# Optimization experiments

Hardware: AMD Instinct MI355X
Metric: run time of the kernel (lower is better)

## Reference

```python
import jax, jax.numpy as jnp
import numpy as np

B, S, H, NH = 4, 2048, 1024, 16
HD = H // NH  # head_size = 64


def setup_inputs() -> dict:
    key = jax.random.key(0)
    ks = jax.random.split(key, 12)
    s = 1.0 / np.sqrt(H)
    return {
        "query": jax.random.normal(ks[0], (B, S, H), jnp.float32),
        "key": jax.random.normal(ks[1], (B, S, H), jnp.float32),
        "value": jax.random.normal(ks[2], (B, S, H), jnp.float32),
        "attention_mask": jax.random.randint(ks[3], (B, 1, S, S), 0, 2).astype(jnp.float32),
        "Wq": jax.random.normal(ks[4], (H, H), jnp.float32) * s,
        "bq": jnp.zeros((H,), jnp.float32),
        "Wk": jax.random.normal(ks[5], (H, H), jnp.float32) * s,
        "bk": jnp.zeros((H,), jnp.float32),
        "Wv": jax.random.normal(ks[6], (H, H), jnp.float32) * s,
        "bv": jnp.zeros((H,), jnp.float32),
        "Wo": jax.random.normal(ks[7], (H, H), jnp.float32) * s,
        "bo": jnp.zeros((H,), jnp.float32),
    }


def reference(query, key, value, attention_mask, Wq, bq, Wk, bk, Wv, bv, Wo, bo):
    # Linear projections (weights stored [in, out])
    q = query @ Wq + bq   # [B, S, H]
    k = key @ Wk + bk
    v = value @ Wv + bv
    # split heads -> [B, NH, S, HD]
    def heads(x):
        return x.reshape(B, -1, NH, HD).transpose(0, 2, 1, 3)
    q, k, v = heads(q), heads(k), heads(v)
    scale = 1.0 / np.sqrt(HD)
    scores = jnp.einsum("bhqd,bhkd->bhqk", q, k) * scale  # [B, NH, S, S]
    scores = scores + attention_mask * (-1e9)
    attn = jax.nn.softmax(scores, axis=-1)
    # dropout is identity in eval mode (deterministic reference)
    out = jnp.einsum("bhqk,bhkd->bhqd", attn, v)  # [B, NH, S, HD]
    out = out.transpose(0, 2, 1, 3).reshape(B, -1, H)  # [B, S, H]
    return out @ Wo + bo
```

## Files before the change

### kernel.cpp

```cpp
#include <hip/hip_runtime.h>
#include <hip/hip_bf16.h>
#include <stdint.h>

#define B_ 4
#define S_ 2048
#define H_ 1024
#define NH_ 16
#define HD_ 64

typedef __attribute__((ext_vector_type(8))) short short8;
typedef __attribute__((ext_vector_type(4))) float f32x4;
typedef __attribute__((ext_vector_type(4))) unsigned short ushort4v;

__device__ __forceinline__ unsigned short f2bf(float f) {
  union { float f; unsigned u; } x; x.f = f;
  unsigned r = x.u + 0x7fffu + ((x.u >> 16) & 1u);
  return (unsigned short)(r >> 16);
}

#define ALDS16(g, l) \
  __builtin_amdgcn_global_load_lds((const __attribute__((address_space(1))) void*)(g), \
                                   (__attribute__((address_space(3))) void*)(l), 16, 0, 0)

__global__ __launch_bounds__(256) void cvt_in(
    const float* __restrict__ q, const float* __restrict__ k, const float* __restrict__ v,
    unsigned short* __restrict__ oq, unsigned short* __restrict__ ok2, unsigned short* __restrict__ ov) {
  const int z = blockIdx.z;
  const float* src = z == 0 ? q : (z == 1 ? k : v);
  unsigned short* dst = z == 0 ? oq : (z == 1 ? ok2 : ov);
  const size_t i = ((size_t)blockIdx.x * 256 + threadIdx.x) * 8;
  const f32x4 a = *reinterpret_cast<const f32x4*>(src + i);
  const f32x4 c = *reinterpret_cast<const f32x4*>(src + i + 4);
  short8 o;
#pragma unroll
  for (int j = 0; j < 4; ++j) { o[j] = (short)f2bf(a[j]); o[j + 4] = (short)f2bf(c[j]); }
  *reinterpret_cast<short8*>(dst + i) = o;
}

__global__ __launch_bounds__(256) void packmask(
    const float* __restrict__ mask, unsigned long long* __restrict__ mb) {
  const int w = threadIdx.x >> 6, lane = threadIdx.x & 63;
  const int wbase = (blockIdx.x * 4 + w) * 32;
#pragma unroll 8
  for (int i = 0; i < 32; ++i) {
    const float v = mask[(size_t)(wbase + i) * 64 + lane];
    const unsigned long long bits = __ballot(v == 0.0f);
    if (lane == 0) mb[wbase + i] = bits;
  }
}

__global__ __launch_bounds__(256) void cvt_w(
    const float* __restrict__ Wq, const float* __restrict__ Wk,
    const float* __restrict__ Wv, const float* __restrict__ Wo,
    unsigned short* __restrict__ wt) {
  __shared__ float tile[64][65];
  const int z = blockIdx.z;
  const float* W = z == 0 ? Wq : (z == 1 ? Wk : (z == 2 ? Wv : Wo));
  unsigned short* out = wt + (size_t)z * H_ * H_;
  const int t = threadIdx.x;
  const int r0 = blockIdx.y * 64, c0 = blockIdx.x * 64;
  const int tr = t >> 4, tc = (t & 15) * 4;
#pragma unroll
  for (int rr = 0; rr < 4; ++rr) {
    const int row = rr * 16 + tr;
    const f32x4 val = *reinterpret_cast<const f32x4*>(W + (size_t)(r0 + row) * H_ + c0 + tc);
#pragma unroll
    for (int j = 0; j < 4; ++j) tile[row][tc + j] = val[j];
  }
  __syncthreads();
#pragma unroll
  for (int rr = 0; rr < 4; ++rr) {
    const int c = rr * 16 + tr;
    ushort4v o;
#pragma unroll
    for (int j = 0; j < 4; ++j) o[j] = f2bf(tile[tc + j][c]);
    *reinterpret_cast<ushort4v*>(out + (size_t)(c0 + c) * H_ + r0 + tc) = o;
  }
}

template <int OUTMODE>
__device__ __forceinline__ void gemm_body(
    const unsigned short* __restrict__ X, const unsigned short* __restrict__ Wt,
    const float* __restrict__ bias, float oscale, unsigned short* __restrict__ obf,
    float* __restrict__ of32) {
  __shared__ unsigned short As[128 * 64];
  __shared__ unsigned short Bs[128 * 64];
  const int t = threadIdx.x;
  const int w = t >> 6, l = t & 63;
  const int lr = l & 15, lg = l >> 4;
  const int brow = blockIdx.x * 128, bcol = blockIdx.y * 128;
  const int wr = (w >> 1) * 64, wc = (w & 1) * 64;
  f32x4 acc[4][4] = {};
  const unsigned short* xb = X + (size_t)brow * 1024;
  const unsigned short* wb = Wt + (size_t)bcol * 1024;
  int srow[4], skl[4];
#pragma unroll
  for (int j = 0; j < 4; ++j) {
    const int c = t + j * 256;
    srow[j] = c >> 3;
    skl[j] = ((c & 7) ^ ((c >> 3) & 7)) * 8;
  }
  for (int kt = 0; kt < 1024; kt += 64) {
#pragma unroll
    for (int j = 0; j < 4; ++j) {
      ALDS16(xb + (size_t)srow[j] * 1024 + kt + skl[j], As + (t + j * 256) * 8);
      ALDS16(wb + (size_t)srow[j] * 1024 + kt + skl[j], Bs + (t + j * 256) * 8);
    }
    __syncthreads();
#pragma unroll
    for (int kk = 0; kk < 2; ++kk) {
      short8 af[4], bf[4];
#pragma unroll
      for (int m = 0; m < 4; ++m) {
        const int ra = wr + m * 16 + lr;
        af[m] = *reinterpret_cast<const short8*>(As + ra * 64 + ((kk * 4 + lg) ^ (ra & 7)) * 8);
      }
#pragma unroll
      for (int n = 0; n < 4; ++n) {
        const int rb = wc + n * 16 + lr;
        bf[n] = *reinterpret_cast<const short8*>(Bs + rb * 64 + ((kk * 4 + lg) ^ (rb & 7)) * 8);
      }
#pragma unroll
      for (int m = 0; m < 4; ++m)
#pragma unroll
        for (int n = 0; n < 4; ++n)
          acc[m][n] = __builtin_amdgcn_mfma_f32_16x16x32_bf16(af[m], bf[n], acc[m][n], 0, 0, 0);
    }
    __syncthreads();
  }
#pragma unroll
  for (int m = 0; m < 4; ++m) {
#pragma unroll
    for (int n = 0; n < 4; ++n) {
#pragma unroll
      for (int r = 0; r < 4; ++r) {
        const int gr = brow + wr + m * 16 + lg * 4 + r;
        const int gc = bcol + wc + n * 16 + lr;
        const float val = (acc[m][n][r] + bias[gc]) * oscale;
        if (OUTMODE == 0) {
          const int bb = gr >> 11, ss = gr & 2047, hh = gc >> 6, dd = gc & 63;
          obf[(((size_t)(bb * NH_ + hh)) * S_ + ss) * HD_ + dd] = f2bf(val);
        } else {
          of32[(size_t)gr * H_ + gc] = val;
        }
      }
    }
  }
}

#define QSCL 0.1803368801111244f

__global__ __launch_bounds__(256, 4) void gemm_qkv(
    const unsigned short* __restrict__ xq, const unsigned short* __restrict__ xk,
    const unsigned short* __restrict__ xv, const unsigned short* __restrict__ wt,
    const float* __restrict__ bq, const float* __restrict__ bk, const float* __restrict__ bv,
    unsigned short* __restrict__ qh, unsigned short* __restrict__ kh,
    unsigned short* __restrict__ vh) {
  const int z = blockIdx.z;
  const unsigned short* X = z == 0 ? xq : (z == 1 ? xk : xv);
  const unsigned short* W = wt + (size_t)z * H_ * H_;
  const float* bias = z == 0 ? bq : (z == 1 ? bk : bv);
  unsigned short* out = z == 0 ? qh : (z == 1 ? kh : vh);
  const float scl = z == 0 ? QSCL : 1.0f;
  gemm_body<0>(X, W, bias, scl, out, nullptr);
}

__global__ __launch_bounds__(256, 4) void gemm_out(
    const unsigned short* __restrict__ ao, const unsigned short* __restrict__ wt,
    const float* __restrict__ bo, float* __restrict__ out) {
  gemm_body<1>(ao, wt, bo, 1.0f, nullptr, out);
}

__global__ __launch_bounds__(256) void vtrans(
    const unsigned short* __restrict__ vh, unsigned short* __restrict__ vt) {
  __shared__ unsigned short tile[64 * 72];
  const int bh = blockIdx.y;
  const int s0 = blockIdx.x * 64;
  const int t = threadIdx.x;
  const unsigned short* src = vh + (size_t)bh * S_ * HD_ + (size_t)s0 * HD_;
#pragma unroll
  for (int r = 0; r < 2; ++r) {
    const int i = t + r * 256;
    const int row = i >> 3, kc = i & 7;
    const short8 v = *reinterpret_cast<const short8*>(src + row * 64 + kc * 8);
    *reinterpret_cast<short8*>(tile + row * 72 + kc * 8) = v;
  }
  __syncthreads();
  unsigned short* dst = vt + (size_t)bh * HD_ * S_;
#pragma unroll
  for (int r = 0; r < 2; ++r) {
    const int i = t + r * 256;
    const int d = i >> 3, sc = i & 7;
    short8 o;
#pragma unroll
    for (int j = 0; j < 8; ++j) o[j] = (short)tile[(sc * 8 + j) * 72 + d];
    *reinterpret_cast<short8*>(dst + (size_t)d * S_ + s0 + sc * 8) = o;
  }
}

__global__ __launch_bounds__(256, 2) void attn_kernel(
    const unsigned short* __restrict__ qh, const unsigned short* __restrict__ kh,
    const unsigned short* __restrict__ vt, const unsigned long long* __restrict__ mb,
    unsigned short* __restrict__ ao) {
  __shared__ unsigned short Ks[2][64 * 64];
  __shared__ unsigned short Vs[2][64 * 64];
  __shared__ unsigned short Ps[4][16 * 64 * 3];
  const int t = threadIdx.x, w = t >> 6, l = t & 63;
  const int lr = l & 15, lg = l >> 4;
  const int flat = blockIdx.x;
  const int g = flat >> 9;
  const int x = flat & 511;
  const int bh = g * 32 + (x & 7) * 4 + (x >> 7);
  const int qt = (x >> 3) & 15;
  const int b = bh >> 4, h = bh & 15;
  const unsigned short* qptr = qh + (size_t)bh * S_ * HD_;
  const unsigned short* kptr = kh + (size_t)bh * S_ * HD_;
  const unsigned short* vptr = vt + (size_t)bh * HD_ * S_;
  const unsigned long long* mbase = mb + (size_t)b * S_ * (S_ / 64);
  const int qbase = qt * 128 + w * 32;

  short8 qf[2][2];
#pragma unroll
  for (int qs = 0; qs < 2; ++qs) {
    const unsigned short* qp = qptr + (size_t)(qbase + qs * 16 + lr) * HD_ + lg * 8;
    qf[qs][0] = *reinterpret_cast<const short8*>(qp);
    qf[qs][1] = *reinterpret_cast<const short8*>(qp + 32);
  }
  short8 ones;
#pragma unroll
  for (int jj = 0; jj < 8; ++jj) ones[jj] = (short)0x3F80;

  const int si0 = t, si1 = t + 256;
  const int srow0 = si0 >> 3, sk0 = ((si0 & 7) ^ (srow0 & 7)) * 8;
  const int srow1 = si1 >> 3, sk1 = ((si1 & 7) ^ (srow1 & 7)) * 8;
  const unsigned short* ksrc0 = kptr + (size_t)srow0 * HD_ + sk0;
  const unsigned short* ksrc1 = kptr + (size_t)srow1 * HD_ + sk1;
  const unsigned short* vsrc0 = vptr + (size_t)srow0 * S_ + sk0;
  const unsigned short* vsrc1 = vptr + (size_t)srow1 * S_ + sk1;
  size_t moff[2][4];
#pragma unroll
  for (int qs = 0; qs < 2; ++qs)
#pragma unroll
    for (int r = 0; r < 4; ++r)
      moff[qs][r] = (size_t)(qbase + qs * 16 + lg * 4 + r) * (S_ / 64);

  ALDS16(ksrc0, Ks[0] + si0 * 8);
  ALDS16(ksrc1, Ks[0] + si1 * 8);
  ALDS16(vsrc0, Vs[0] + si0 * 8);
  ALDS16(vsrc1, Vs[0] + si1 * 8);
  __syncthreads();

  f32x4 acc_o[2][4] = {};
  f32x4 acc_l[2] = {};
  unsigned short* pw = Ps[w];
  int cur = 0;

  for (int kv = 0; kv < S_; kv += 64) {
    unsigned msel[2][4][4];
#pragma unroll
    for (int qs = 0; qs < 2; ++qs)
#pragma unroll
      for (int r = 0; r < 4; ++r) {
        const unsigned long long mwv = mbase[moff[qs][r] + (kv >> 6)];
        const unsigned long long sh = mwv >> lr;
        const unsigned lo = (unsigned)sh, hi = (unsigned)(sh >> 32);
        msel[qs][r][0] = 0u - (lo & 1u);
        msel[qs][r][1] = 0u - ((lo >> 16) & 1u);
        msel[qs][r][2] = 0u - (hi & 1u);
        msel[qs][r][3] = 0u - ((hi >> 16) & 1u);
      }

    const int nkv = (kv + 64 < S_) ? kv + 64 : 0;
    ALDS16(ksrc0 + (size_t)nkv * HD_, Ks[cur ^ 1] + si0 * 8);
    ALDS16(ksrc1 + (size_t)nkv * HD_, Ks[cur ^ 1] + si1 * 8);
    ALDS16(vsrc0 + nkv, Vs[cur ^ 1] + si0 * 8);
    ALDS16(vsrc1 + nkv, Vs[cur ^ 1] + si1 * 8);

    float p[2][4][4];
#pragma unroll
    for (int n = 0; n < 4; ++n) {
      const int krow = n * 16 + lr;
      const short8 kf0 = *reinterpret_cast<const short8*>(Ks[cur] + krow * 64 + ((0 + lg) ^ (krow & 7)) * 8);
      const short8 kf1 = *reinterpret_cast<const short8*>(Ks[cur] + krow * 64 + ((4 + lg) ^ (krow & 7)) * 8);
#pragma unroll
      for (int qs = 0; qs < 2; ++qs) {
        f32x4 sc = {};
        sc = __builtin_amdgcn_mfma_f32_16x16x32_bf16(qf[qs][0], kf0, sc, 0, 0, 0);
        sc = __builtin_amdgcn_mfma_f32_16x16x32_bf16(qf[qs][1], kf1, sc, 0, 0, 0);
#pragma unroll
        for (int r = 0; r < 4; ++r) {
          union { float f; unsigned u; } cv;
          cv.f = __builtin_amdgcn_exp2f(sc[r]);
          cv.u &= msel[qs][r][n];
          p[qs][n][r] = cv.f;
        }
      }
    }

    short8 pf[2][2];
#pragma unroll
    for (int qs = 0; qs < 2; ++qs) {
#pragma unroll
      for (int r = 0; r < 4; ++r) {
        const int row = lg * 4 + r;
#pragma unroll
        for (int n = 0; n < 4; ++n) {
          union { float f; unsigned u; } cv; cv.f = p[qs][n][r];
          const int col = n * 16 + lr;
          pw[row * 64 + ((col >> 3) ^ (row & 7)) * 8 + (col & 7)] = (unsigned short)(cv.u >> 16);
        }
      }
      pf[qs][0] = *reinterpret_cast<const short8*>(pw + lr * 64 + ((0 + lg) ^ (lr & 7)) * 8);
      pf[qs][1] = *reinterpret_cast<const short8*>(pw + lr * 64 + ((4 + lg) ^ (lr & 7)) * 8);
      acc_l[qs] = __builtin_amdgcn_mfma_f32_16x16x32_bf16(pf[qs][0], ones, acc_l[qs], 0, 0, 0);
      acc_l[qs] = __builtin_amdgcn_mfma_f32_16x16x32_bf16(pf[qs][1], ones, acc_l[qs], 0, 0, 0);
    }

    __builtin_amdgcn_s_setprio(1);
#pragma unroll
    for (int d = 0; d < 4; ++d) {
      const int vrow = d * 16 + lr;
      const short8 vf0 = *reinterpret_cast<const short8*>(Vs[cur] + vrow * 64 + ((0 + lg) ^ (vrow & 7)) * 8);
      const short8 vf1 = *reinterpret_cast<const short8*>(Vs[cur] + vrow * 64 + ((4 + lg) ^ (vrow & 7)) * 8);
#pragma unroll
      for (int qs = 0; qs < 2; ++qs) {
        acc_o[qs][d] = __builtin_amdgcn_mfma_f32_16x16x32_bf16(pf[qs][0], vf0, acc_o[qs][d], 0, 0, 0);
        acc_o[qs][d] = __builtin_amdgcn_mfma_f32_16x16x32_bf16(pf[qs][1], vf1, acc_o[qs][d], 0, 0, 0);
      }
    }
    __builtin_amdgcn_s_setprio(0);
    __syncthreads();
    cur ^= 1;
  }

#pragma unroll
  for (int qs = 0; qs < 2; ++qs)
#pragma unroll
    for (int r = 0; r < 4; ++r) {
      const float inv = __builtin_amdgcn_rcpf(acc_l[qs][r]);
      const int qrow = qbase + qs * 16 + lg * 4 + r;
      unsigned short* orow = ao + ((size_t)b * S_ + qrow) * H_ + h * HD_;
#pragma unroll
      for (int d = 0; d < 4; ++d)
        orow[d * 16 + lr] = f2bf(acc_o[qs][d][r] * inv);
    }
}

extern "C" void kernel_launch(void* const* d_in, const int* in_sizes, int n_in,
                              void* d_out, int out_size, void* d_ws, size_t ws_size,
                              hipStream_t stream) {
  (void)in_sizes; (void)n_in; (void)out_size; (void)ws_size;
  const float* query = (const float*)d_in[0];
  const float* key_  = (const float*)d_in[1];
  const float* value = (const float*)d_in[2];
  const float* mask  = (const float*)d_in[3];
  const float* Wq = (const float*)d_in[4];
  const float* bq = (const float*)d_in[5];
  const float* Wk = (const float*)d_in[6];
  const float* bk = (const float*)d_in[7];
  const float* Wv = (const float*)d_in[8];
  const float* bv = (const float*)d_in[9];
  const float* Wo = (const float*)d_in[10];
  const float* bo = (const float*)d_in[11];
  float* out = (float*)d_out;

  char* ws = (char*)d_ws;
  const size_t MB16 = (size_t)1 << 24;
  unsigned short* XQ = (unsigned short*)(ws + 0 * MB16);
  unsigned short* XK = (unsigned short*)(ws + 1 * MB16);
  unsigned short* XV = (unsigned short*)(ws + 2 * MB16);
  unsigned short* QH = (unsigned short*)(ws + 3 * MB16);
  unsigned short* KH = (unsigned short*)(ws + 4 * MB16);
  unsigned short* VH = (unsigned short*)(ws + 5 * MB16);
  unsigned short* WT = (unsigned short*)(ws + 6 * MB16);
  unsigned long long* MBits = (unsigned long long*)(ws + 6 * MB16 + (size_t)4 * H_ * H_ * 2);
  unsigned short* AO = XQ;
  unsigned short* VT = XK;

  cvt_in<<<dim3(4096, 1, 3), 256, 0, stream>>>(query, key_, value, XQ, XK, XV);
  packmask<<<dim3(2048), 256, 0, stream>>>(mask, MBits);
  cvt_w<<<dim3(16, 16, 4), 256, 0, stream>>>(Wq, Wk, Wv, Wo, WT);
  gemm_qkv<<<dim3(64, 8, 3), 256, 0, stream>>>(XQ, XK, XV, WT, bq, bk, bv, QH, KH, VH);
  vtrans<<<dim3(32, 64), 256, 0, stream>>>(VH, VT);
  attn_kernel<<<dim3(1024), 256, 0, stream>>>(QH, KH, VT, MBits, AO);
  gemm_out<<<dim3(64, 8, 1), 256, 0, stream>>>(AO, WT + 3 * (size_t)H_ * H_, bo, out);
}
```

Measured before the change: 266.2 us.

## Triple-buffer K/V tiles in attention with two-ahead prefetch and partial vmcnt wait

The attention kernel moves from double to triple buffering of its K and V LDS tiles. Each tile is now prefetched two iterations ahead, and the full __syncthreads is replaced by an s_waitcnt vmcnt(4) plus barrier, so the newest prefetch can stay in flight across the barrier. The oversized P scratch buffer is cut to one third, which keeps total LDS use unchanged and so does not reduce occupancy. The aim is to hide global-to-LDS load latency better, at the cost of relying on exact vmcnt ordering, since the mask loads are also counted as vector memory operations.

```diff
diff --git a/kernel.cpp b/kernel.cpp
--- a/kernel.cpp
+++ b/kernel.cpp
@@ -202,9 +202,9 @@
     const unsigned short* __restrict__ qh, const unsigned short* __restrict__ kh,
     const unsigned short* __restrict__ vt, const unsigned long long* __restrict__ mb,
     unsigned short* __restrict__ ao) {
-  __shared__ unsigned short Ks[2][64 * 64];
-  __shared__ unsigned short Vs[2][64 * 64];
-  __shared__ unsigned short Ps[4][16 * 64 * 3];
+  __shared__ unsigned short Ks[3][64 * 64];
+  __shared__ unsigned short Vs[3][64 * 64];
+  __shared__ unsigned short Ps[4][16 * 64];
   const int t = threadIdx.x, w = t >> 6, l = t & 63;
   const int lr = l & 15, lg = l >> 4;
   const int flat = blockIdx.x;
@@ -248,7 +248,13 @@
   ALDS16(ksrc1, Ks[0] + si1 * 8);
   ALDS16(vsrc0, Vs[0] + si0 * 8);
   ALDS16(vsrc1, Vs[0] + si1 * 8);
-  __syncthreads();
+  ALDS16(ksrc0 + (size_t)64 * HD_, Ks[1] + si0 * 8);
+  ALDS16(ksrc1 + (size_t)64 * HD_, Ks[1] + si1 * 8);
+  ALDS16(vsrc0 + 64, Vs[1] + si0 * 8);
+  ALDS16(vsrc1 + 64, Vs[1] + si1 * 8);
+  asm volatile("s_waitcnt vmcnt(4)");
+  __builtin_amdgcn_s_barrier();
+  __builtin_amdgcn_sched_barrier(0);
 
   f32x4 acc_o[2][4] = {};
   f32x4 acc_l[2] = {};
@@ -270,18 +276,22 @@
         msel[qs][r][3] = 0u - ((hi >> 16) & 1u);
       }
 
-    const int nkv = (kv + 64 < S_) ? kv + 64 : 0;
-    ALDS16(ksrc0 + (size_t)nkv * HD_, Ks[cur ^ 1] + si0 * 8);
-    ALDS16(ksrc1 + (size_t)nkv * HD_, Ks[cur ^ 1] + si1 * 8);
-    ALDS16(vsrc0 + nkv, Vs[cur ^ 1] + si0 * 8);
-    ALDS16(vsrc1 + nkv, Vs[cur ^ 1] + si1 * 8);
+    const int stb = (cur == 0) ? 2 : cur - 1;
+    const int nkv = (kv + 128 < S_) ? kv + 128 : kv + 128 - S_;
+    ALDS16(ksrc0 + (size_t)nkv * HD_, Ks[stb] + si0 * 8);
+    ALDS16(ksrc1 + (size_t)nkv * HD_, Ks[stb] + si1 * 8);
+    ALDS16(vsrc0 + nkv, Vs[stb] + si0 * 8);
+    ALDS16(vsrc1 + nkv, Vs[stb] + si1 * 8);
+
+    const unsigned short* Kc = Ks[cur];
+    const unsigned short* Vc = Vs[cur];
 
     float p[2][4][4];
 #pragma unroll
     for (int n = 0; n < 4; ++n) {
       const int krow = n * 16 + lr;
-      const short8 kf0 = *reinterpret_cast<const short8*>(Ks[cur] + krow * 64 + ((0 + lg) ^ (krow & 7)) * 8);
-      const short8 kf1 = *reinterpret_cast<const short8*>(Ks[cur] + krow * 64 + ((4 + lg) ^ (krow & 7)) * 8);
+      const short8 kf0 = *reinterpret_cast<const short8*>(Kc + krow * 64 + ((0 + lg) ^ (krow & 7)) * 8);
+      const short8 kf1 = *reinterpret_cast<const short8*>(Kc + krow * 64 + ((4 + lg) ^ (krow & 7)) * 8);
 #pragma unroll
       for (int qs = 0; qs < 2; ++qs) {
         f32x4 sc = {};
@@ -320,8 +330,8 @@
 #pragma unroll
     for (int d = 0; d < 4; ++d) {
       const int vrow = d * 16 + lr;
-      const short8 vf0 = *reinterpret_cast<const short8*>(Vs[cur] + vrow * 64 + ((0 + lg) ^ (vrow & 7)) * 8);
-      const short8 vf1 = *reinterpret_cast<const short8*>(Vs[cur] + vrow * 64 + ((4 + lg) ^ (vrow & 7)) * 8);
+      const short8 vf0 = *reinterpret_cast<const short8*>(Vc + vrow * 64 + ((0 + lg) ^ (vrow & 7)) * 8);
+      const short8 vf1 = *reinterpret_cast<const short8*>(Vc + vrow * 64 + ((4 + lg) ^ (vrow & 7)) * 8);
 #pragma unroll
       for (int qs = 0; qs < 2; ++qs) {
         acc_o[qs][d] = __builtin_amdgcn_mfma_f32_16x16x32_bf16(pf[qs][0], vf0, acc_o[qs][d], 0, 0, 0);
@@ -329,8 +339,11 @@
       }
     }
     __builtin_amdgcn_s_setprio(0);
-    __syncthreads();
-    cur ^= 1;
+
+    asm volatile("s_waitcnt vmcnt(4)");
+    __builtin_amdgcn_s_barrier();
+    __builtin_amdgcn_sched_barrier(0);
+    cur = (cur == 2) ? 0 : cur + 1;
   }
 
 #pragma unroll
```

After: 267.6 us. About the same (+0.5%).

## Fuse V transpose into V projection epilogue and halve attention query tile

Applied to the files above, without the earlier changes.

The V projection now gets its own GEMM launch whose epilogue writes V directly in transposed [B,NH,HD,S] layout using 4-wide stores, which removes the separate vtrans kernel and one round trip of V through memory. The attention kernel drops from 32 to 16 query rows per wave (64 per block), doubling the grid to 2048 blocks, shrinking the P scratch buffer, and raising the launch-bounds occupancy hint to 4. The block-to-head mapping is reworked so that consecutive blocks spread across XCDs. The trade-off is that each K/V tile loaded into LDS is now reused by fewer query rows, so K/V traffic per unit of work doubles.

```diff
diff --git a/kernel.cpp b/kernel.cpp
--- a/kernel.cpp
+++ b/kernel.cpp
@@ -132,16 +132,25 @@
   for (int m = 0; m < 4; ++m) {
 #pragma unroll
     for (int n = 0; n < 4; ++n) {
-#pragma unroll
-      for (int r = 0; r < 4; ++r) {
-        const int gr = brow + wr + m * 16 + lg * 4 + r;
-        const int gc = bcol + wc + n * 16 + lr;
-        const float val = (acc[m][n][r] + bias[gc]) * oscale;
-        if (OUTMODE == 0) {
-          const int bb = gr >> 11, ss = gr & 2047, hh = gc >> 6, dd = gc & 63;
-          obf[(((size_t)(bb * NH_ + hh)) * S_ + ss) * HD_ + dd] = f2bf(val);
-        } else {
-          of32[(size_t)gr * H_ + gc] = val;
+      const int gr0 = brow + wr + m * 16 + lg * 4;
+      const int gc = bcol + wc + n * 16 + lr;
+      if (OUTMODE == 2) {
+        ushort4v o;
+#pragma unroll
+        for (int r = 0; r < 4; ++r) o[r] = f2bf((acc[m][n][r] + bias[gc]) * oscale);
+        const int bb = gr0 >> 11, ss = gr0 & 2047, hh = gc >> 6, dd = gc & 63;
+        *reinterpret_cast<ushort4v*>(obf + ((size_t)(bb * NH_ + hh) * HD_ + dd) * S_ + ss) = o;
+      } else {
+#pragma unroll
+        for (int r = 0; r < 4; ++r) {
+          const int gr = gr0 + r;
+          const float val = (acc[m][n][r] + bias[gc]) * oscale;
+          if (OUTMODE == 0) {
+            const int bb = gr >> 11, ss = gr & 2047, hh = gc >> 6, dd = gc & 63;
+            obf[(((size_t)(bb * NH_ + hh)) * S_ + ss) * HD_ + dd] = f2bf(val);
+          } else {
+            of32[(size_t)gr * H_ + gc] = val;
+          }
         }
       }
     }
@@ -152,17 +161,22 @@
 
 __global__ __launch_bounds__(256, 4) void gemm_qkv(
     const unsigned short* __restrict__ xq, const unsigned short* __restrict__ xk,
-    const unsigned short* __restrict__ xv, const unsigned short* __restrict__ wt,
-    const float* __restrict__ bq, const float* __restrict__ bk, const float* __restrict__ bv,
-    unsigned short* __restrict__ qh, unsigned short* __restrict__ kh,
-    unsigned short* __restrict__ vh) {
+    const unsigned short* __restrict__ wt,
+    const float* __restrict__ bq, const float* __restrict__ bk,
+    unsigned short* __restrict__ qh, unsigned short* __restrict__ kh) {
   const int z = blockIdx.z;
-  const unsigned short* X = z == 0 ? xq : (z == 1 ? xk : xv);
+  const unsigned short* X = z == 0 ? xq : xk;
   const unsigned short* W = wt + (size_t)z * H_ * H_;
-  const float* bias = z == 0 ? bq : (z == 1 ? bk : bv);
-  unsigned short* out = z == 0 ? qh : (z == 1 ? kh : vh);
+  const float* bias = z == 0 ? bq : bk;
+  unsigned short* out = z == 0 ? qh : kh;
   const float scl = z == 0 ? QSCL : 1.0f;
   gemm_body<0>(X, W, bias, scl, out, nullptr);
+}
+
+__global__ __launch_bounds__(256, 4) void gemm_v(
+    const unsigned short* __restrict__ xv, const unsigned short* __restrict__ wt,
+    const float* __restrict__ bv, unsigned short* __restrict__ vtv) {
+  gemm_body<2>(xv, wt + (size_t)2 * H_ * H_, bv, 1.0f, vtv, nullptr);
 }
 
 __global__ __launch_bounds__(256, 4) void gemm_out(
@@ -171,60 +185,33 @@
   gemm_body<1>(ao, wt, bo, 1.0f, nullptr, out);
 }
 
-__global__ __launch_bounds__(256) void vtrans(
-    const unsigned short* __restrict__ vh, unsigned short* __restrict__ vt) {
-  __shared__ unsigned short tile[64 * 72];
-  const int bh = blockIdx.y;
-  const int s0 = blockIdx.x * 64;
-  const int t = threadIdx.x;
-  const unsigned short* src = vh + (size_t)bh * S_ * HD_ + (size_t)s0 * HD_;
-#pragma unroll
-  for (int r = 0; r < 2; ++r) {
-    const int i = t + r * 256;
-    const int row = i >> 3, kc = i & 7;
-    const short8 v = *reinterpret_cast<const short8*>(src + row * 64 + kc * 8);
-    *reinterpret_cast<short8*>(tile + row * 72 + kc * 8) = v;
-  }
-  __syncthreads();
-  unsigned short* dst = vt + (size_t)bh * HD_ * S_;
-#pragma unroll
-  for (int r = 0; r < 2; ++r) {
-    const int i = t + r * 256;
-    const int d = i >> 3, sc = i & 7;
-    short8 o;
-#pragma unroll
-    for (int j = 0; j < 8; ++j) o[j] = (short)tile[(sc * 8 + j) * 72 + d];
-    *reinterpret_cast<short8*>(dst + (size_t)d * S_ + s0 + sc * 8) = o;
-  }
-}
-
-__global__ __launch_bounds__(256, 2) void attn_kernel(
+__global__ __launch_bounds__(256, 4) void attn_kernel(
     const unsigned short* __restrict__ qh, const unsigned short* __restrict__ kh,
     const unsigned short* __restrict__ vt, const unsigned long long* __restrict__ mb,
     unsigned short* __restrict__ ao) {
   __shared__ unsigned short Ks[2][64 * 64];
   __shared__ unsigned short Vs[2][64 * 64];
-  __shared__ unsigned short Ps[4][16 * 64 * 3];
+  __shared__ unsigned short Ps[4][16 * 64];
   const int t = threadIdx.x, w = t >> 6, l = t & 63;
   const int lr = l & 15, lg = l >> 4;
   const int flat = blockIdx.x;
-  const int g = flat >> 9;
-  const int x = flat & 511;
-  const int bh = g * 32 + (x & 7) * 4 + (x >> 7);
-  const int qt = (x >> 3) & 15;
+  const int xcd = flat & 7;
+  const int gen = flat >> 10;
+  const int hh = (flat >> 8) & 3;
+  const int qt = (flat >> 3) & 31;
+  const int bh = gen * 32 + xcd * 4 + hh;
   const int b = bh >> 4, h = bh & 15;
   const unsigned short* qptr = qh + (size_t)bh * S_ * HD_;
   const unsigned short* kptr = kh + (size_t)bh * S_ * HD_;
   const unsigned short* vptr = vt + (size_t)bh * HD_ * S_;
   const unsigned long long* mbase = mb + (size_t)b * S_ * (S_ / 64);
-  const int qbase = qt * 128 + w * 32;
-
-  short8 qf[2][2];
-#pragma unroll
-  for (int qs = 0; qs < 2; ++qs) {
-    const unsigned short* qp = qptr + (size_t)(qbase + qs * 16 + lr) * HD_ + lg * 8;
-    qf[qs][0] = *reinterpret_cast<const short8*>(qp);
-    qf[qs][1] = *reinterpret_cast<const short8*>(qp + 32);
+  const int qbase = qt * 64 + w * 16;
+
+  short8 qf[2];
+  {
+    const unsigned short* qp = qptr + (size_t)(qbase + lr) * HD_ + lg * 8;
+    qf[0] = *reinterpret_cast<const short8*>(qp);
+    qf[1] = *reinterpret_cast<const short8*>(qp + 32);
   }
   short8 ones;
 #pragma unroll
@@ -237,12 +224,10 @@
   const unsigned short* ksrc1 = kptr + (size_t)srow1 * HD_ + sk1;
   const unsigned short* vsrc0 = vptr + (size_t)srow0 * S_ + sk0;
   const unsigned short* vsrc1 = vptr + (size_t)srow1 * S_ + sk1;
-  size_t moff[2][4];
-#pragma unroll
-  for (int qs = 0; qs < 2; ++qs)
-#pragma unroll
-    for (int r = 0; r < 4; ++r)
-      moff[qs][r] = (size_t)(qbase + qs * 16 + lg * 4 + r) * (S_ / 64);
+  size_t moff[4];
+#pragma unroll
+  for (int r = 0; r < 4; ++r)
+    moff[r] = (size_t)(qbase + lg * 4 + r) * (S_ / 64);
 
   ALDS16(ksrc0, Ks[0] + si0 * 8);
   ALDS16(ksrc1, Ks[0] + si1 * 8);
@@ -250,25 +235,23 @@
   ALDS16(vsrc1, Vs[0] + si1 * 8);
   __syncthreads();
 
-  f32x4 acc_o[2][4] = {};
-  f32x4 acc_l[2] = {};
+  f32x4 acc_o[4] = {};
+  f32x4 acc_l = {};
   unsigned short* pw = Ps[w];
   int cur = 0;
 
   for (int kv = 0; kv < S_; kv += 64) {
-    unsigned msel[2][4][4];
-#pragma unroll
-    for (int qs = 0; qs < 2; ++qs)
-#pragma unroll
-      for (int r = 0; r < 4; ++r) {
-        const unsigned long long mwv = mbase[moff[qs][r] + (kv >> 6)];
-        const unsigned long long sh = mwv >> lr;
-        const unsigned lo = (unsigned)sh, hi = (unsigned)(sh >> 32);
-        msel[qs][r][0] = 0u - (lo & 1u);
-        msel[qs][r][1] = 0u - ((lo >> 16) & 1u);
-        msel[qs][r][2] = 0u - (hi & 1u);
-        msel[qs][r][3] = 0u - ((hi >> 16) & 1u);
-      }
+    unsigned msel[4][4];
+#pragma unroll
+    for (int r = 0; r < 4; ++r) {
+      const unsigned long long mwv = mbase[moff[r] + (kv >> 6)];
+      const unsigned long long sh = mwv >> lr;
+      const unsigned lo = (unsigned)sh, hi = (unsigned)(sh >> 32);
+      msel[r][0] = 0u - (lo & 1u);
+      msel[r][1] = 0u - ((lo >> 16) & 1u);
+      msel[r][2] = 0u - (hi & 1u);
+      msel[r][3] = 0u - ((hi >> 16) & 1u);
+    }
 
     const int nkv = (kv + 64 < S_) ? kv + 64 : 0;
     ALDS16(ksrc0 + (size_t)nkv * HD_, Ks[cur ^ 1] + si0 * 8);
@@ -276,57 +259,50 @@
     ALDS16(vsrc0 + nkv, Vs[cur ^ 1] + si0 * 8);
     ALDS16(vsrc1 + nkv, Vs[cur ^ 1] + si1 * 8);
 
-    float p[2][4][4];
+    const unsigned short* Kc = Ks[cur];
+    const unsigned short* Vc = Vs[cur];
+
+    float p[4][4];
 #pragma unroll
     for (int n = 0; n < 4; ++n) {
       const int krow = n * 16 + lr;
-      const short8 kf0 = *reinterpret_cast<const short8*>(Ks[cur] + krow * 64 + ((0 + lg) ^ (krow & 7)) * 8);
-      const short8 kf1 = *reinterpret_cast<const short8*>(Ks[cur] + krow * 64 + ((4 + lg) ^ (krow & 7)) * 8);
-#pragma unroll
-      for (int qs = 0; qs < 2; ++qs) {
-        f32x4 sc = {};
-        sc = __builtin_amdgcn_mfma_f32_16x16x32_bf16(qf[qs][0], kf0, sc, 0, 0, 0);
-        sc = __builtin_amdgcn_mfma_f32_16x16x32_bf16(qf[qs][1], kf1, sc, 0, 0, 0);
-#pragma unroll
-        for (int r = 0; r < 4; ++r) {
-          union { float f; unsigned u; } cv;
-          cv.f = __builtin_amdgcn_exp2f(sc[r]);
-          cv.u &= msel[qs][r][n];
-          p[qs][n][r] = cv.f;
-        }
-      }
-    }
-
-    short8 pf[2][2];
-#pragma unroll
-    for (int qs = 0; qs < 2; ++qs) {
+      const short8 kf0 = *reinterpret_cast<const short8*>(Kc + krow * 64 + ((0 + lg) ^ (krow & 7)) * 8);
+      const short8 kf1 = *reinterpret_cast<const short8*>(Kc + krow * 64 + ((4 + lg) ^ (krow & 7)) * 8);
+      f32x4 sc = {};
+      sc = __builtin_amdgcn_mfma_f32_16x16x32_bf16(qf[0], kf0, sc, 0, 0, 0);
+      sc = __builtin_amdgcn_mfma_f32_16x16x32_bf16(qf[1], kf1, sc, 0, 0, 0);
 #pragma unroll
       for (int r = 0; r < 4; ++r) {
-        const int row = lg * 4 + r;
-#pragma unroll
-        for (int n = 0; n < 4; ++n) {
-          union { float f; unsigned u; } cv; cv.f = p[qs][n][r];
-          const int col = n * 16 + lr;
-          pw[row * 64 + ((col >> 3) ^ (row & 7)) * 8 + (col & 7)] = (unsigned short)(cv.u >> 16);
-        }
-      }
-      pf[qs][0] = *reinterpret_cast<const short8*>(pw + lr * 64 + ((0 + lg) ^ (lr & 7)) * 8);
-      pf[qs][1] = *reinterpret_cast<const short8*>(pw + lr * 64 + ((4 + lg) ^ (lr & 7)) * 8);
-      acc_l[qs] = __builtin_amdgcn_mfma_f32_16x16x32_bf16(pf[qs][0], ones, acc_l[qs], 0, 0, 0);
-      acc_l[qs] = __builtin_amdgcn_mfma_f32_16x16x32_bf16(pf[qs][1], ones, acc_l[qs], 0, 0, 0);
-    }
+        union { float f; unsigned u; } cv;
+        cv.f = __builtin_amdgcn_exp2f(sc[r]);
+        cv.u &= msel[r][n];
+        p[n][r] = cv.f;
+      }
+    }
+
+#pragma unroll
+    for (int r = 0; r < 4; ++r) {
+      const int row = lg * 4 + r;
+#pragma unroll
+      for (int n = 0; n < 4; ++n) {
+        union { float f; unsigned u; } cv; cv.f = p[n][r];
+        const int col = n * 16 + lr;
+        pw[row * 64 + ((col >> 3) ^ (row & 7)) * 8 + (col & 7)] = (unsigned short)(cv.u >> 16);
+      }
+    }
+    short8 pf0 = *reinterpret_cast<const short8*>(pw + lr * 64 + ((0 + lg) ^ (lr & 7)) * 8);
+    short8 pf1 = *reinterpret_cast<const short8*>(pw + lr * 64 + ((4 + lg) ^ (lr & 7)) * 8);
+    acc_l = __builtin_amdgcn_mfma_f32_16x16x32_bf16(pf0, ones, acc_l, 0, 0, 0);
+    acc_l = __builtin_amdgcn_mfma_f32_16x16x32_bf16(pf1, ones, acc_l, 0, 0, 0);
 
     __builtin_amdgcn_s_setprio(1);
 #pragma unroll
     for (int d = 0; d < 4; ++d) {
       const int vrow = d * 16 + lr;
-      const short8 vf0 = *reinterpret_cast<const short8*>(Vs[cur] + vrow * 64 + ((0 + lg) ^ (vrow & 7)) * 8);
-      const short8 vf1 = *reinterpret_cast<const short8*>(Vs[cur] + vrow * 64 + ((4 + lg) ^ (vrow & 7)) * 8);
-#pragma unroll
-      for (int qs = 0; qs < 2; ++qs) {
-        acc_o[qs][d] = __builtin_amdgcn_mfma_f32_16x16x32_bf16(pf[qs][0], vf0, acc_o[qs][d], 0, 0, 0);
-        acc_o[qs][d] = __builtin_amdgcn_mfma_f32_16x16x32_bf16(pf[qs][1], vf1, acc_o[qs][d], 0, 0, 0);
-      }
+      const short8 vf0 = *reinterpret_cast<const short8*>(Vc + vrow * 64 + ((0 + lg) ^ (vrow & 7)) * 8);
+      const short8 vf1 = *reinterpret_cast<const short8*>(Vc + vrow * 64 + ((4 + lg) ^ (vrow & 7)) * 8);
+      acc_o[d] = __builtin_amdgcn_mfma_f32_16x16x32_bf16(pf0, vf0, acc_o[d], 0, 0, 0);
+      acc_o[d] = __builtin_amdgcn_mfma_f32_16x16x32_bf16(pf1, vf1, acc_o[d], 0, 0, 0);
     }
     __builtin_amdgcn_s_setprio(0);
     __syncthreads();
@@ -334,16 +310,14 @@
   }
 
 #pragma unroll
-  for (int qs = 0; qs < 2; ++qs)
-#pragma unroll
-    for (int r = 0; r < 4; ++r) {
-      const float inv = __builtin_amdgcn_rcpf(acc_l[qs][r]);
-      const int qrow = qbase + qs * 16 + lg * 4 + r;
-      unsigned short* orow = ao + ((size_t)b * S_ + qrow) * H_ + h * HD_;
-#pragma unroll
-      for (int d = 0; d < 4; ++d)
-        orow[d * 16 + lr] = f2bf(acc_o[qs][d][r] * inv);
-    }
+  for (int r = 0; r < 4; ++r) {
+    const float inv = __builtin_amdgcn_rcpf(acc_l[r]);
+    const int qrow = qbase + lg * 4 + r;
+    unsigned short* orow = ao + ((size_t)b * S_ + qrow) * H_ + h * HD_;
+#pragma unroll
+    for (int d = 0; d < 4; ++d)
+      orow[d * 16 + lr] = f2bf(acc_o[d][r] * inv);
+  }
 }
 
 extern "C" void kernel_launch(void* const* d_in, const int* in_sizes, int n_in,
@@ -371,17 +345,16 @@
   unsigned short* XV = (unsigned short*)(ws + 2 * MB16);
   unsigned short* QH = (unsigned short*)(ws + 3 * MB16);
   unsigned short* KH = (unsigned short*)(ws + 4 * MB16);
-  unsigned short* VH = (unsigned short*)(ws + 5 * MB16);
+  unsigned short* VT = (unsigned short*)(ws + 5 * MB16);
   unsigned short* WT = (unsigned short*)(ws + 6 * MB16);
   unsigned long long* MBits = (unsigned long long*)(ws + 6 * MB16 + (size_t)4 * H_ * H_ * 2);
   unsigned short* AO = XQ;
-  unsigned short* VT = XK;
 
   cvt_in<<<dim3(4096, 1, 3), 256, 0, stream>>>(query, key_, value, XQ, XK, XV);
   packmask<<<dim3(2048), 256, 0, stream>>>(mask, MBits);
   cvt_w<<<dim3(16, 16, 4), 256, 0, stream>>>(Wq, Wk, Wv, Wo, WT);
-  gemm_qkv<<<dim3(64, 8, 3), 256, 0, stream>>>(XQ, XK, XV, WT, bq, bk, bv, QH, KH, VH);
-  vtrans<<<dim3(32, 64), 256, 0, stream>>>(VH, VT);
-  attn_kernel<<<dim3(1024), 256, 0, stream>>>(QH, KH, VT, MBits, AO);
+  gemm_qkv<<<dim3(64, 8, 2), 256, 0, stream>>>(XQ, XK, WT, bq, bk, QH, KH);
+  gemm_v<<<dim3(64, 8), 256, 0, stream>>>(XV, WT, bv, VT);
+  attn_kernel<<<dim3(2048), 256, 0, stream>>>(QH, KH, VT, MBits, AO);
   gemm_out<<<dim3(64, 8, 1), 256, 0, stream>>>(AO, WT + 3 * (size_t)H_ * H_, bo, out);
 }
```

Result: faster. 257.0 us (-3.5%).
